# Kernel optimization log

Hardware: AMD Instinct MI355X
Metric: run time of the kernel (lower is better)

## Reference

```python
import jax, jax.numpy as jnp
import numpy as np

B, L, D, DEPTH, FF, VOCAB = 2, 2048, 1024, 4, 4096, 32000

def setup_inputs():
    key = jax.random.key(0)
    ks = jax.random.split(key, 16)
    n = lambda k, s, sc: jax.random.normal(k, s, dtype=jnp.float32) * sc
    sw = 0.01 / float(np.sqrt(D))  # xavier_normal with gain 0.01 on square dims
    return dict(
        tokens=jax.random.randint(ks[0], (B, L), 0, VOCAB),
        emb=n(ks[1], (VOCAB, D), 0.02),
        Wz=n(ks[2], (DEPTH, D, D), sw), bz=jnp.zeros((DEPTH, D)),
        Wza=n(ks[3], (DEPTH, D, D), sw), bza=jnp.zeros((DEPTH, D)),
        Wy=n(ks[4], (DEPTH, D, D), sw), by=jnp.zeros((DEPTH, D)),
        Wya=n(ks[5], (DEPTH, D, D), sw), bya=jnp.zeros((DEPTH, D)),
        lc_re=n(ks[6], (DEPTH, D), 1.0), lc_im=n(ks[7], (DEPTH, D), 1.0),
        g_in=jnp.ones((DEPTH, D)), g_sc=jnp.ones((DEPTH, D)), g_ffn=jnp.ones((DEPTH, D)),
        Wf=n(ks[8], (DEPTH, D, FF), 0.02), bf=jnp.zeros((DEPTH, FF)),
        Wfa=n(ks[9], (DEPTH, D, FF), 0.02), bfa=jnp.zeros((DEPTH, FF)),
        Wfo=n(ks[10], (DEPTH, FF, D), 0.02), bfo=jnp.zeros((DEPTH, D)),
        ln_w=jnp.ones((D,)), ln_b=jnp.zeros((D,)),
        Wout=n(ks[11], (D, VOCAB), 0.02), bout=jnp.zeros((VOCAB,)),
    )

def _silu(x):
    return x * jax.nn.sigmoid(x)

def _rms(x, w, eps=1e-6):
    return x * jax.lax.rsqrt(jnp.mean(x * x, axis=-1, keepdims=True) + eps) * w

def reference(tokens, emb, Wz, bz, Wza, bza, Wy, by, Wya, bya, lc_re, lc_im,
              g_in, g_sc, g_ffn, Wf, bf, Wfa, bfa, Wfo, bfo, ln_w, ln_b, Wout, bout):
    Bq, Lq = tokens.shape
    # Embedding with max_norm=1: torch renorms accessed rows to norm <= 1
    e = emb[tokens]
    nrm = jnp.linalg.norm(e, axis=-1, keepdims=True)
    x = e * jnp.minimum(1.0, 1.0 / jnp.maximum(nrm, 1e-7))
    # Decaying phazor kernel (shared across layers; phazor_angle_scale is a fixed buffer)
    angle = jnp.power(0.001, jnp.linspace(0.0, 1.0, D))
    ln_ph = (1e-5 + 1j * angle).astype(jnp.complex64)      # [D]
    t = jnp.arange(Lq, dtype=jnp.float32)
    ph = jnp.exp(t[:, None] * ln_ph[None, :])              # [L, D] complex
    pf = jnp.fft.fft(ph, n=2 * Lq, axis=0)                 # [2L, D]
    decay = jnp.exp(ln_ph)                                 # [D]
    for i in range(DEPTH):
        # --- SConv sublayer (pre-RMSNorm + residual) ---
        xr = x
        xn = _rms(x, g_sc[i])
        z = (xn @ Wz[i] + bz[i]) * _silu(xn @ Wza[i] + bza[i])
        zf = jnp.fft.fft(z.astype(jnp.complex64), n=2 * Lq, axis=1)
        h = jnp.fft.ifft(zf * pf[None], axis=1)[:, :Lq]    # inner-chunk causal decaying conv
        lc = (lc_re[i] + 1j * lc_im[i]).astype(jnp.complex64)
        h = h + lc[None, None, :] * ph[None] * decay[None, None, :]  # cross-chunk state carry
        y = (_rms(h.real, g_in[i]) @ Wy[i] + by[i]) * _silu(xn @ Wya[i] + bya[i])
        x = xr + y
        # --- FFN SwiGLU sublayer (pre-RMSNorm + residual) ---
        xr = x
        xn = _rms(x, g_ffn[i])
        x = xr + ((xn @ Wf[i] + bf[i]) * _silu(xn @ Wfa[i] + bfa[i])) @ Wfo[i] + bfo[i]
    # Final LayerNorm + vocab projection
    mu = jnp.mean(x, axis=-1, keepdims=True)
    var = jnp.mean((x - mu) ** 2, axis=-1, keepdims=True)
    x = (x - mu) * jax.lax.rsqrt(var + 1e-5) * ln_w + ln_b
    return x @ Wout + bout
```

## Files before the change

kernel.cpp:

```cpp
#include <hip/hip_runtime.h>
#include <math.h>

typedef __attribute__((ext_vector_type(8))) short bf16x8;
typedef __attribute__((ext_vector_type(4))) float f32x4;

#define DEVI __device__ __forceinline__

DEVI short f2bf(float f) {
  unsigned u = __builtin_bit_cast(unsigned, f);
  return (short)((u + 0x7fffu + ((u >> 16) & 1u)) >> 16);
}
DEVI float bf2f(short s) {
  unsigned u = ((unsigned)(unsigned short)s) << 16;
  return __builtin_bit_cast(float, u);
}

DEVI float silu_f(float v) { return v / (1.0f + expf(-v)); }

DEVI void async16(const void* g, void* l) {
  __builtin_amdgcn_global_load_lds(
      (const __attribute__((address_space(1))) void*)g,
      (__attribute__((address_space(3))) void*)l, 16, 0, 0);
}

template <int N>
DEVI void waitvm() { asm volatile("s_waitcnt vmcnt(%0)" ::"i"(N) : "memory"); }
DEVI void barrier_mem() { asm volatile("s_barrier" ::: "memory"); }
DEVI void lgkm0_sb() {
  asm volatile("s_waitcnt lgkmcnt(0)" ::: "memory");
  __builtin_amdgcn_sched_barrier(0);
}

template <int NROWT>
DEVI void tile_map(int* bx, int* by) {
  const int nwg = gridDim.x;
  const int lin = blockIdx.x;
  const int q = nwg >> 3;
  const int wgid = (lin & 7) * q + (lin >> 3);
  *by = wgid % NROWT;
  *bx = wgid / NROWT;
}

#define SWZ(r) ((ks ^ (((r) >> 1) & 3)) << 4)

__global__ __launch_bounds__(512, 2) void gemm8_k(const short* __restrict__ A,
                                                  const short* __restrict__ BT,
                                                  const float* __restrict__ bias,
                                                  float* __restrict__ outp,
                                                  int N, int K) {
  __shared__ __align__(16) char lds[2 * 65536];
  int bx, by;
  tile_map<16>(&bx, &by);
  const int row0 = by << 8, col0 = bx << 8;
  const int t = threadIdx.x, w = t >> 6, lane = t & 63;
  const int wm = w >> 2, wn = w & 3;
  const int lr = lane & 15, ks = lane >> 4;
  f32x4 acc[8][4] = {};

  const int sslot = (t & 3) ^ ((t >> 3) & 3);
  const char* gA = (const char*)A + ((size_t)(row0 + (t >> 2)) * K) * 2 + sslot * 16;
  const char* gB = (const char*)BT + ((size_t)(col0 + (t >> 2)) * K) * 2 + sslot * 16;
  const size_t cstep = (size_t)K << 8;
  const int t16 = t << 4;

  const int nkt = K >> 6;

#define SA8(nb, kt, s)                                                        \
  {                                                                           \
    const size_t co = (size_t)(kt) * 128 + (s) * 64;                          \
    async16(gA + co, (nb) + (s) * 16384 + t16);                               \
    async16(gA + cstep + co, (nb) + (s) * 16384 + 8192 + t16);                \
  }
#define SB8(nb, kt, s)                                                        \
  {                                                                           \
    const size_t co = (size_t)(kt) * 128 + (s) * 64;                          \
    async16(gB + co, (nb) + 32768 + (s) * 16384 + t16);                       \
    async16(gB + cstep + co, (nb) + 32768 + (s) * 16384 + 8192 + t16);        \
  }
#define RB8(s)                                                                \
  _Pragma("unroll") for (int n = 0; n < 4; ++n) {                             \
    const int rb = (wn << 6) + (n << 4) + lr;                                 \
    bfr[n] = *(const bf16x8*)(base + 32768 + (s) * 16384 + rb * 64 + SWZ(rb)); \
  }
#define RA8(s, mh)                                                            \
  _Pragma("unroll") for (int m = 0; m < 4; ++m) {                             \
    const int r = (wm << 7) + (mh) * 64 + (m << 4) + lr;                      \
    af[m] = *(const bf16x8*)(base + (s) * 16384 + r * 64 + SWZ(r));           \
  }
#define MM8(mh)                                                               \
  __builtin_amdgcn_s_setprio(1);                                              \
  _Pragma("unroll") for (int m = 0; m < 4; ++m)                               \
  _Pragma("unroll") for (int n = 0; n < 4; ++n)                               \
      acc[(mh) * 4 + m][n] = __builtin_amdgcn_mfma_f32_16x16x32_bf16(         \
          af[m], bfr[n], acc[(mh) * 4 + m][n], 0, 0, 0);                      \
  __builtin_amdgcn_s_setprio(0);                                              \
  __builtin_amdgcn_sched_barrier(0);

  {
    char* nb = lds;
    SA8(nb, 0, 0); SB8(nb, 0, 0); SA8(nb, 0, 1); SB8(nb, 0, 1);
  }

  for (int kt = 0; kt < nkt; ++kt) {
    const int ktn = kt + 1;
    const char* base = lds + (kt & 1) * 65536;
    char* nb = lds + (ktn & 1) * 65536;
    bf16x8 af[4], bfr[4];
    waitvm<4>();
    barrier_mem();
    if (ktn < nkt) SA8(nb, ktn, 0);
    RB8(0); RA8(0, 0);
    lgkm0_sb();
    MM8(0);
    barrier_mem();
    if (ktn < nkt) SB8(nb, ktn, 0);
    RA8(0, 1);
    lgkm0_sb();
    MM8(1);
    if (ktn < nkt) waitvm<4>();
    else waitvm<0>();
    barrier_mem();
    if (ktn < nkt) SA8(nb, ktn, 1);
    RB8(1); RA8(1, 0);
    lgkm0_sb();
    MM8(0);
    barrier_mem();
    if (ktn < nkt) SB8(nb, ktn, 1);
    RA8(1, 1);
    lgkm0_sb();
    MM8(1);
  }

  const int orow = row0 + (wm << 7) + (ks << 2);
  const int ocol = col0 + (wn << 6) + lr;
#pragma unroll
  for (int mf = 0; mf < 8; ++mf) {
#pragma unroll
    for (int n = 0; n < 4; ++n) {
      const int c = ocol + (n << 4);
      const float bv = bias[c];
#pragma unroll
      for (int i = 0; i < 4; ++i) {
        const int r = orow + (mf << 4) + i;
        outp[(size_t)r * N + c] = acc[mf][n][i] + bv;
      }
    }
  }
#undef SA8
#undef SB8
#undef RB8
#undef RA8
#undef MM8
}

__global__ __launch_bounds__(512, 2) void dual8_k(const short* __restrict__ A,
                                                  const short* __restrict__ BT1,
                                                  const short* __restrict__ BT2,
                                                  const float* __restrict__ bias1,
                                                  const float* __restrict__ bias2,
                                                  short* __restrict__ outp,
                                                  int N, int K) {
  __shared__ __align__(16) char lds[2 * 32768];
  int bx, by;
  tile_map<16>(&bx, &by);
  const int row0 = by << 8, col0 = bx << 7;
  const int t = threadIdx.x, w = t >> 6, lane = t & 63;
  const int wm = w >> 1, wn = w & 1;
  const int lr = lane & 15, ks = lane >> 4;
  f32x4 acc1[4][4] = {}, acc2[4][4] = {};

  const int sslot = (t & 3) ^ ((t >> 3) & 3);
  const char* gA = (const char*)A + ((size_t)(row0 + (t >> 2)) * K) * 2 + sslot * 16;
  const char* gB1 = (const char*)BT1 + ((size_t)(col0 + (t >> 2)) * K) * 2 + sslot * 16;
  const char* gB2 = (const char*)BT2 + ((size_t)(col0 + (t >> 2)) * K) * 2 + sslot * 16;
  const size_t cstep = (size_t)K << 8;
  const int t16 = t << 4;
  const int nkt = K >> 5;

#define SAD(nb, kt)                                                           \
  {                                                                           \
    const size_t co = (size_t)(kt) * 64;                                      \
    async16(gA + co, (nb) + t16);                                             \
    async16(gA + cstep + co, (nb) + 8192 + t16);                              \
  }
#define SB1D(nb, kt) async16(gB1 + (size_t)(kt) * 64, (nb) + 16384 + t16)
#define SB2D(nb, kt) async16(gB2 + (size_t)(kt) * 64, (nb) + 24576 + t16)

  { char* nb = lds; SAD(nb, 0); SB1D(nb, 0); SB2D(nb, 0); }

  for (int kt = 0; kt < nkt; ++kt) {
    const int ktn = kt + 1;
    const char* base = lds + (kt & 1) * 32768;
    char* nb = lds + (ktn & 1) * 32768;
    bf16x8 af[4], bfr[4];
    waitvm<1>();
    barrier_mem();
    if (ktn < nkt) { SAD(nb, ktn); SB1D(nb, ktn); }
#pragma unroll
    for (int n = 0; n < 4; ++n) {
      const int rb = (wn << 6) + (n << 4) + lr;
      bfr[n] = *(const bf16x8*)(base + 16384 + rb * 64 + SWZ(rb));
    }
#pragma unroll
    for (int m = 0; m < 4; ++m) {
      const int r = (wm << 6) + (m << 4) + lr;
      af[m] = *(const bf16x8*)(base + r * 64 + SWZ(r));
    }
    lgkm0_sb();
    __builtin_amdgcn_s_setprio(1);
#pragma unroll
    for (int m = 0; m < 4; ++m)
#pragma unroll
      for (int n = 0; n < 4; ++n)
        acc1[m][n] = __builtin_amdgcn_mfma_f32_16x16x32_bf16(af[m], bfr[n], acc1[m][n], 0, 0, 0);
    __builtin_amdgcn_s_setprio(0);
    __builtin_amdgcn_sched_barrier(0);
    if (ktn < nkt) waitvm<3>();
    else waitvm<0>();
    barrier_mem();
    if (ktn < nkt) SB2D(nb, ktn);
#pragma unroll
    for (int n = 0; n < 4; ++n) {
      const int rb = (wn << 6) + (n << 4) + lr;
      bfr[n] = *(const bf16x8*)(base + 24576 + rb * 64 + SWZ(rb));
    }
    lgkm0_sb();
    __builtin_amdgcn_s_setprio(1);
#pragma unroll
    for (int m = 0; m < 4; ++m)
#pragma unroll
      for (int n = 0; n < 4; ++n)
        acc2[m][n] = __builtin_amdgcn_mfma_f32_16x16x32_bf16(af[m], bfr[n], acc2[m][n], 0, 0, 0);
    __builtin_amdgcn_s_setprio(0);
    __builtin_amdgcn_sched_barrier(0);
  }

  const int orow = row0 + (wm << 6) + (ks << 2);
  const int ocol = col0 + (wn << 6) + lr;
#pragma unroll
  for (int m = 0; m < 4; ++m) {
#pragma unroll
    for (int n = 0; n < 4; ++n) {
      const int c = ocol + (n << 4);
      const float bv1 = bias1[c], bv2 = bias2[c];
#pragma unroll
      for (int i = 0; i < 4; ++i) {
        const int r = orow + (m << 4) + i;
        outp[(size_t)r * N + c] = f2bf((acc1[m][n][i] + bv1) * silu_f(acc2[m][n][i] + bv2));
      }
    }
  }
#undef SAD
#undef SB1D
#undef SB2D
}

__global__ __launch_bounds__(256, 2) void triple_k(const short* __restrict__ A,
                                                   const short* __restrict__ BT1,
                                                   const short* __restrict__ BT2,
                                                   const short* __restrict__ BT3,
                                                   const float* __restrict__ b1,
                                                   const float* __restrict__ b2,
                                                   const float* __restrict__ b3,
                                                   short* __restrict__ zout,
                                                   short* __restrict__ yaout,
                                                   int N, int K) {
  constexpr int PBB = 28672;
  __shared__ __align__(16) char lds[2 * PBB];
  int bx, by;
  tile_map<64>(&bx, &by);
  const int row0 = by << 6, col0 = bx << 7;
  const int t = threadIdx.x, w = t >> 6, lane = t & 63;
  const int wr = w >> 1, wc = w & 1;
  const int lr = lane & 15, ks = lane >> 4;
  f32x4 acc1[2][4] = {}, acc2[2][4] = {}, acc3[2][4] = {};

  const int sslot = (t & 3) ^ ((t >> 3) & 3);
  const char* gA = (const char*)A + ((size_t)(row0 + (t >> 2)) * K) * 2 + sslot * 16;
  const size_t brow = ((size_t)(col0 + (t >> 2)) * K) * 2 + sslot * 16;
  const char* gB1 = (const char*)BT1 + brow;
  const char* gB2 = (const char*)BT2 + brow;
  const char* gB3 = (const char*)BT3 + brow;
  const size_t cstep = (size_t)K * 128;
  const int t16 = t << 4;
  const int nkt = K >> 5;

#define STA(nb, kt) async16(gA + (size_t)(kt) * 64, (nb) + t16)
#define STB(nb, kt, gp, off)                                                  \
  {                                                                           \
    const size_t co = (size_t)(kt) * 64;                                      \
    async16((gp) + co, (nb) + (off) + t16);                                   \
    async16((gp) + cstep + co, (nb) + (off) + 4096 + t16);                    \
  }

  { char* nb = lds; STA(nb, 0); STB(nb, 0, gB1, 4096); STB(nb, 0, gB2, 12288); STB(nb, 0, gB3, 20480); }

  for (int kt = 0; kt < nkt; ++kt) {
    const int ktn = kt + 1;
    const char* base = lds + (kt & 1) * PBB;
    char* nb = lds + (ktn & 1) * PBB;
    bf16x8 af[2], bfr[4];
    waitvm<0>();
    barrier_mem();
    if (ktn < nkt) { STA(nb, ktn); STB(nb, ktn, gB1, 4096); }
#pragma unroll
    for (int m = 0; m < 2; ++m) {
      const int r = (wr << 5) + (m << 4) + lr;
      af[m] = *(const bf16x8*)(base + r * 64 + SWZ(r));
    }
#pragma unroll
    for (int n = 0; n < 4; ++n) {
      const int rb = (wc << 6) + (n << 4) + lr;
      bfr[n] = *(const bf16x8*)(base + 4096 + rb * 64 + SWZ(rb));
    }
    lgkm0_sb();
    __builtin_amdgcn_s_setprio(1);
#pragma unroll
    for (int m = 0; m < 2; ++m)
#pragma unroll
      for (int n = 0; n < 4; ++n)
        acc1[m][n] = __builtin_amdgcn_mfma_f32_16x16x32_bf16(af[m], bfr[n], acc1[m][n], 0, 0, 0);
    __builtin_amdgcn_s_setprio(0);
    __builtin_amdgcn_sched_barrier(0);
    if (ktn < nkt) STB(nb, ktn, gB2, 12288);
#pragma unroll
    for (int n = 0; n < 4; ++n) {
      const int rb = (wc << 6) + (n << 4) + lr;
      bfr[n] = *(const bf16x8*)(base + 12288 + rb * 64 + SWZ(rb));
    }
    lgkm0_sb();
    __builtin_amdgcn_s_setprio(1);
#pragma unroll
    for (int m = 0; m < 2; ++m)
#pragma unroll
      for (int n = 0; n < 4; ++n)
        acc2[m][n] = __builtin_amdgcn_mfma_f32_16x16x32_bf16(af[m], bfr[n], acc2[m][n], 0, 0, 0);
    __builtin_amdgcn_s_setprio(0);
    __builtin_amdgcn_sched_barrier(0);
    if (ktn < nkt) STB(nb, ktn, gB3, 20480);
#pragma unroll
    for (int n = 0; n < 4; ++n) {
      const int rb = (wc << 6) + (n << 4) + lr;
      bfr[n] = *(const bf16x8*)(base + 20480 + rb * 64 + SWZ(rb));
    }
    lgkm0_sb();
    __builtin_amdgcn_s_setprio(1);
#pragma unroll
    for (int m = 0; m < 2; ++m)
#pragma unroll
      for (int n = 0; n < 4; ++n)
        acc3[m][n] = __builtin_amdgcn_mfma_f32_16x16x32_bf16(af[m], bfr[n], acc3[m][n], 0, 0, 0);
    __builtin_amdgcn_s_setprio(0);
    __builtin_amdgcn_sched_barrier(0);
  }

  const int orow = row0 + (wr << 5) + (ks << 2);
  const int ocol = col0 + (wc << 6) + lr;
#pragma unroll
  for (int m = 0; m < 2; ++m) {
#pragma unroll
    for (int n = 0; n < 4; ++n) {
      const int c = ocol + (n << 4);
      const float bv1 = b1[c], bv2 = b2[c], bv3 = b3[c];
#pragma unroll
      for (int i = 0; i < 4; ++i) {
        const int r = orow + (m << 4) + i;
        const size_t idx = (size_t)r * N + c;
        zout[idx] = f2bf((acc1[m][n][i] + bv1) * silu_f(acc2[m][n][i] + bv2));
        yaout[idx] = f2bf(acc3[m][n][i] + bv3);
      }
    }
  }
#undef STA
#undef STB
}

template <int MODE, int BM, int BN, int WM, int WN, int NBUF>
__global__ __launch_bounds__(256, 2) void gemm_k(const short* __restrict__ A,
                                                 const short* __restrict__ BT,
                                                 const float* __restrict__ bias,
                                                 const short* __restrict__ aux,
                                                 void* __restrict__ outp,
                                                 int N, int K) {
  constexpr int MF = WM / 16, NF = WN / 16;
  constexpr int NWN = BN / WN;
  constexpr int PBB = (BM + BN) * 64;
  constexpr int DEPTH = NBUF - 1;
  constexpr int L = (BM + BN) / 64;
  static_assert((BM / WM) * (BN / WN) == 4, "4 waves");
  __shared__ __align__(16) char lds[NBUF * PBB];
  int bx, by;
  tile_map<4096 / BM>(&bx, &by);
  const int row0 = by * BM, col0 = bx * BN;
  const int t = threadIdx.x, w = t >> 6, lane = t & 63;
  const int wr = w / NWN, wc = w % NWN;
  f32x4 acc[MF][NF] = {};

  const int sslot = (t & 3) ^ ((t >> 3) & 3);
  const char* gA0 = (const char*)A + ((size_t)(row0 + (t >> 2)) * K) * 2 + sslot * 16;
  const char* gB0 = (const char*)BT + ((size_t)(col0 + (t >> 2)) * K) * 2 + sslot * 16;
  const size_t ccstep = (size_t)K * 128;
  const int wb = w << 10;
  const int lr = lane & 15, ks = lane >> 4;

  const int NIT = K >> 5;
  auto stage = [&](int buf, int it) {
    char* dst = lds + buf * PBB;
    const size_t io = (size_t)it * 64;
#pragma unroll
    for (int cc = 0; cc < BM / 64; ++cc)
      async16(gA0 + io + cc * ccstep, dst + cc * 4096 + wb);
#pragma unroll
    for (int cc = 0; cc < BN / 64; ++cc)
      async16(gB0 + io + cc * ccstep, dst + BM * 64 + cc * 4096 + wb);
  };

#pragma unroll
  for (int pit = 0; pit < DEPTH; ++pit) stage(pit, pit);

  for (int it = 0; it < NIT; ++it) {
    const int rem = NIT - it;
    if (rem >= DEPTH + 1) waitvm<L * (DEPTH - 1)>();
    else if (rem >= 2) waitvm<L>();
    else waitvm<0>();
    barrier_mem();
    if (it + DEPTH < NIT) stage((it + DEPTH) % NBUF, it + DEPTH);
    const char* base = lds + (it % NBUF) * PBB;
    bf16x8 af[MF], bfr[NF];
#pragma unroll
    for (int m = 0; m < MF; ++m) {
      const int r = wr * WM + m * 16 + lr;
      af[m] = *(const bf16x8*)(base + r * 64 + SWZ(r));
    }
#pragma unroll
    for (int n = 0; n < NF; ++n) {
      const int r = wc * WN + n * 16 + lr;
      bfr[n] = *(const bf16x8*)(base + BM * 64 + r * 64 + SWZ(r));
    }
    lgkm0_sb();
    __builtin_amdgcn_s_setprio(1);
#pragma unroll
    for (int m = 0; m < MF; ++m)
#pragma unroll
      for (int n = 0; n < NF; ++n)
        acc[m][n] = __builtin_amdgcn_mfma_f32_16x16x32_bf16(af[m], bfr[n], acc[m][n], 0, 0, 0);
    __builtin_amdgcn_s_setprio(0);
    __builtin_amdgcn_sched_barrier(0);
  }

  const int orow = row0 + wr * WM + (ks << 2);
  const int ocol = col0 + wc * WN + lr;
#pragma unroll
  for (int m = 0; m < MF; ++m) {
#pragma unroll
    for (int n = 0; n < NF; ++n) {
      const int c = ocol + (n << 4);
      const float bv = bias[c];
#pragma unroll
      for (int i = 0; i < 4; ++i) {
        const int r = orow + (m << 4) + i;
        const size_t idx = (size_t)r * N + c;
        float v = acc[m][n][i] + bv;
        if (MODE == 0) ((float*)outp)[idx] = v;
        else if (MODE == 3) ((float*)outp)[idx] += v * silu_f(bf2f(aux[idx]));
        else ((float*)outp)[idx] += v;
      }
    }
  }
}

__global__ __launch_bounds__(256) void transp_k(const float* __restrict__ W,
                                                short* __restrict__ WT,
                                                int R, int C) {
  __shared__ float tile[32][33];
  const size_t moff = (size_t)blockIdx.z * R * C;
  const float* Wp = W + moff;
  short* Tp = WT + moff;
  const int c0 = blockIdx.x << 5, r0 = blockIdx.y << 5;
  const int tx = threadIdx.x, ty = threadIdx.y;
#pragma unroll
  for (int i = 0; i < 4; ++i)
    tile[ty + 8 * i][tx] = Wp[(size_t)(r0 + ty + 8 * i) * C + (c0 + tx)];
  __syncthreads();
#pragma unroll
  for (int i = 0; i < 4; ++i)
    Tp[(size_t)(c0 + ty + 8 * i) * R + (r0 + tx)] = f2bf(tile[tx][ty + 8 * i]);
}

__global__ __launch_bounds__(256) void embed_k(const int* __restrict__ tok,
                                               const float* __restrict__ emb,
                                               float* __restrict__ x) {
  const int row = blockIdx.x, t = threadIdx.x, w = t >> 6, lane = t & 63;
  const int token = tok[row];
  float4 v = ((const float4*)(emb + (size_t)token * 1024))[t];
  float ss = v.x * v.x + v.y * v.y + v.z * v.z + v.w * v.w;
#pragma unroll
  for (int off = 32; off; off >>= 1) ss += __shfl_xor(ss, off, 64);
  __shared__ float red[4];
  if (lane == 0) red[w] = ss;
  __syncthreads();
  const float nrm = sqrtf(red[0] + red[1] + red[2] + red[3]);
  const float sc = fminf(1.0f, 1.0f / fmaxf(nrm, 1e-7f));
  v.x *= sc; v.y *= sc; v.z *= sc; v.w *= sc;
  ((float4*)(x + (size_t)row * 1024))[t] = v;
}

template <int BF>
__global__ __launch_bounds__(256) void rms_k(const void* __restrict__ xin,
                                             const float* __restrict__ g,
                                             short* __restrict__ o) {
  const int row = blockIdx.x, t = threadIdx.x, w = t >> 6, lane = t & 63;
  float v0, v1, v2, v3;
  if (BF) {
    short4 s = ((const short4*)((const short*)xin + (size_t)row * 1024))[t];
    v0 = bf2f(s.x); v1 = bf2f(s.y); v2 = bf2f(s.z); v3 = bf2f(s.w);
  } else {
    float4 v = ((const float4*)((const float*)xin + (size_t)row * 1024))[t];
    v0 = v.x; v1 = v.y; v2 = v.z; v3 = v.w;
  }
  float ss = v0 * v0 + v1 * v1 + v2 * v2 + v3 * v3;
#pragma unroll
  for (int off = 32; off; off >>= 1) ss += __shfl_xor(ss, off, 64);
  __shared__ float red[4];
  if (lane == 0) red[w] = ss;
  __syncthreads();
  const float sc = rsqrtf((red[0] + red[1] + red[2] + red[3]) * (1.0f / 1024.0f) + 1e-6f);
  float4 gv = ((const float4*)g)[t];
  short4 ov = make_short4(f2bf(v0 * sc * gv.x), f2bf(v1 * sc * gv.y),
                          f2bf(v2 * sc * gv.z), f2bf(v3 * sc * gv.w));
  *(short4*)(o + (size_t)row * 1024 + 4 * t) = ov;
}

__global__ __launch_bounds__(256) void ln_k(const float* __restrict__ x,
                                            const float* __restrict__ lw,
                                            const float* __restrict__ lb,
                                            short* __restrict__ o) {
  const int row = blockIdx.x, t = threadIdx.x, w = t >> 6, lane = t & 63;
  float4 v = ((const float4*)(x + (size_t)row * 1024))[t];
  float s1 = v.x + v.y + v.z + v.w;
  float s2 = v.x * v.x + v.y * v.y + v.z * v.z + v.w * v.w;
#pragma unroll
  for (int off = 32; off; off >>= 1) {
    s1 += __shfl_xor(s1, off, 64);
    s2 += __shfl_xor(s2, off, 64);
  }
  __shared__ float red[8];
  if (lane == 0) { red[w] = s1; red[4 + w] = s2; }
  __syncthreads();
  const float mu = (red[0] + red[1] + red[2] + red[3]) * (1.0f / 1024.0f);
  const float ex2 = (red[4] + red[5] + red[6] + red[7]) * (1.0f / 1024.0f);
  const float rs = rsqrtf(ex2 - mu * mu + 1e-5f);
  float4 wv = ((const float4*)lw)[t];
  float4 bv = ((const float4*)lb)[t];
  short4 ov = make_short4(f2bf((v.x - mu) * rs * wv.x + bv.x),
                          f2bf((v.y - mu) * rs * wv.y + bv.y),
                          f2bf((v.z - mu) * rs * wv.z + bv.z),
                          f2bf((v.w - mu) * rs * wv.w + bv.w));
  *(short4*)(o + (size_t)row * 1024 + 4 * t) = ov;
}

DEVI void decay_of(int d, float* dr, float* di) {
  const float ang = powf(1e-3f, (float)d * (1.0f / 1023.0f));
  float sn, cs;
  sincosf(ang, &sn, &cs);
  const float mag = expf(1e-5f);
  *dr = mag * cs; *di = mag * sn;
}

__global__ __launch_bounds__(256) void s1_k(const short* __restrict__ z,
                                            float* __restrict__ Er, float* __restrict__ Ei) {
  const int d = (blockIdx.x << 8) + threadIdx.x;
  const int c = blockIdx.y, b = blockIdx.z;
  float dr, di;
  decay_of(d, &dr, &di);
  const short* zp = z + ((size_t)(b * 2048 + c * 64) << 10) + d;
  float sr = 0.0f, si = 0.0f;
  for (int k = 0; k < 64; ++k) {
    float zv = bf2f(zp[(size_t)k << 10]);
    float nr = dr * sr - di * si + zv;
    si = dr * si + di * sr;
    sr = nr;
  }
  const int idx = ((b << 5) + c) * 1024 + d;
  Er[idx] = sr; Ei[idx] = si;
}

__global__ __launch_bounds__(256) void s3_k(const short* __restrict__ z,
                                            const float* __restrict__ Er,
                                            const float* __restrict__ Ei,
                                            const float* __restrict__ lcre,
                                            const float* __restrict__ lcim,
                                            short* __restrict__ h) {
  const int d = (blockIdx.x << 8) + threadIdx.x;
  const int c = blockIdx.y, b = blockIdx.z;
  float dr, di;
  decay_of(d, &dr, &di);
  float ar = dr, ai = di;
#pragma unroll
  for (int q = 0; q < 6; ++q) { float nr = ar * ar - ai * ai; ai = 2.0f * ar * ai; ar = nr; }
  float sr = 0.0f, si = 0.0f;
  for (int cc = 0; cc < c; ++cc) {
    const int eidx = ((b << 5) + cc) * 1024 + d;
    const float er = Er[eidx], ei = Ei[eidx];
    const float nr = ar * sr - ai * si + er;
    si = ar * si + ai * sr + ei;
    sr = nr;
  }
  float wr = 1.0f, wi = 0.0f, br = ar, bi = ai;
  int e = c;
  while (e) {
    if (e & 1) { float nr = wr * br - wi * bi; wi = wr * bi + wi * br; wr = nr; }
    float nb = br * br - bi * bi; bi = 2.0f * br * bi; br = nb;
    e >>= 1;
  }
  { float nr = wr * dr - wi * di; wi = wr * di + wi * dr; wr = nr; }
  const float lr_ = lcre[d], li_ = lcim[d];
  const size_t base = ((size_t)(b * 2048 + c * 64) << 10) + d;
  for (int k = 0; k < 64; ++k) {
    const float zv = bf2f(z[base + ((size_t)k << 10)]);
    const float nr = dr * sr - di * si + zv;
    si = dr * si + di * sr;
    sr = nr;
    h[base + ((size_t)k << 10)] = f2bf(sr + lr_ * wr - li_ * wi);
    const float nw = wr * dr - wi * di;
    wi = wr * di + wi * dr;
    wr = nw;
  }
}

extern "C" void kernel_launch(void* const* d_in, const int* in_sizes, int n_in,
                              void* d_out, int out_size, void* d_ws, size_t ws_size,
                              hipStream_t stream) {
  const int* tokens = (const int*)d_in[0];
  const float* emb = (const float*)d_in[1];
  const float* Wz = (const float*)d_in[2];
  const float* bz = (const float*)d_in[3];
  const float* Wza = (const float*)d_in[4];
  const float* bza = (const float*)d_in[5];
  const float* Wy = (const float*)d_in[6];
  const float* by = (const float*)d_in[7];
  const float* Wya = (const float*)d_in[8];
  const float* bya = (const float*)d_in[9];
  const float* lc_re = (const float*)d_in[10];
  const float* lc_im = (const float*)d_in[11];
  const float* g_in = (const float*)d_in[12];
  const float* g_sc = (const float*)d_in[13];
  const float* g_ffn = (const float*)d_in[14];
  const float* Wf = (const float*)d_in[15];
  const float* bf = (const float*)d_in[16];
  const float* Wfa = (const float*)d_in[17];
  const float* bfa = (const float*)d_in[18];
  const float* Wfo = (const float*)d_in[19];
  const float* bfo = (const float*)d_in[20];
  const float* ln_w = (const float*)d_in[21];
  const float* ln_b = (const float*)d_in[22];
  const float* Wout = (const float*)d_in[23];
  const float* bout = (const float*)d_in[24];

  char* p = (char*)d_ws;
  float* xb = (float*)p;   p += (size_t)4096 * 1024 * 4;
  short* zb = (short*)p;   p += (size_t)4096 * 1024 * 2;
  short* hb = (short*)p;   p += (size_t)4096 * 1024 * 2;
  short* yab = (short*)p;  p += (size_t)4096 * 1024 * 2;
  float* Er = (float*)p;   p += (size_t)2 * 32 * 1024 * 4;
  float* Ei = (float*)p;   p += (size_t)2 * 32 * 1024 * 4;
  short* xnb = (short*)p;  p += (size_t)4096 * 1024 * 2;
  short* hnb = (short*)p;  p += (size_t)4096 * 1024 * 2;
  short* gb = (short*)p;   p += (size_t)4096 * 4096 * 2;
  short* WzT = (short*)p;  p += (size_t)4 * 1024 * 1024 * 2;
  short* WzaT = (short*)p; p += (size_t)4 * 1024 * 1024 * 2;
  short* WyT = (short*)p;  p += (size_t)4 * 1024 * 1024 * 2;
  short* WyaT = (short*)p; p += (size_t)4 * 1024 * 1024 * 2;
  short* WfT = (short*)p;  p += (size_t)4 * 1024 * 4096 * 2;
  short* WfaT = (short*)p; p += (size_t)4 * 1024 * 4096 * 2;
  short* WfoT = (short*)p; p += (size_t)4 * 1024 * 4096 * 2;
  short* WoutT = (short*)p; p += (size_t)32000 * 1024 * 2;

  const dim3 tb(32, 8);
  transp_k<<<dim3(32, 32, 4), tb, 0, stream>>>(Wz, WzT, 1024, 1024);
  transp_k<<<dim3(32, 32, 4), tb, 0, stream>>>(Wza, WzaT, 1024, 1024);
  transp_k<<<dim3(32, 32, 4), tb, 0, stream>>>(Wy, WyT, 1024, 1024);
  transp_k<<<dim3(32, 32, 4), tb, 0, stream>>>(Wya, WyaT, 1024, 1024);
  transp_k<<<dim3(128, 32, 4), tb, 0, stream>>>(Wf, WfT, 1024, 4096);
  transp_k<<<dim3(128, 32, 4), tb, 0, stream>>>(Wfa, WfaT, 1024, 4096);
  transp_k<<<dim3(32, 128, 4), tb, 0, stream>>>(Wfo, WfoT, 4096, 1024);
  transp_k<<<dim3(1000, 32, 1), tb, 0, stream>>>(Wout, WoutT, 1024, 32000);

  embed_k<<<4096, 256, 0, stream>>>(tokens, emb, xb);

  for (int i = 0; i < 4; ++i) {
    const size_t dd = (size_t)i * 1024 * 1024;
    const size_t dv = (size_t)i * 1024;
    const size_t dw = (size_t)i * 1024 * 4096;
    const size_t df = (size_t)i * 4096;
    rms_k<0><<<4096, 256, 0, stream>>>(xb, g_sc + dv, xnb);
    triple_k<<<512, 256, 0, stream>>>(xnb, WzT + dd, WzaT + dd, WyaT + dd,
                                      bz + dv, bza + dv, bya + dv, zb, yab, 1024, 1024);
    s1_k<<<dim3(4, 32, 2), 256, 0, stream>>>(zb, Er, Ei);
    s3_k<<<dim3(4, 32, 2), 256, 0, stream>>>(zb, Er, Ei, lc_re + dv, lc_im + dv, hb);
    rms_k<1><<<4096, 256, 0, stream>>>(hb, g_in + dv, hnb);
    gemm_k<3, 64, 128, 32, 64, 3><<<512, 256, 0, stream>>>(
        hnb, WyT + dd, by + dv, yab, xb, 1024, 1024);
    rms_k<0><<<4096, 256, 0, stream>>>(xb, g_ffn + dv, xnb);
    dual8_k<<<512, 512, 0, stream>>>(xnb, WfT + dw, WfaT + dw, bf + df, bfa + df,
                                     gb, 4096, 1024);
    gemm_k<4, 64, 128, 32, 64, 4><<<512, 256, 0, stream>>>(
        gb, WfoT + dw, bfo + dv, nullptr, xb, 1024, 4096);
  }

  ln_k<<<4096, 256, 0, stream>>>(xb, ln_w, ln_b, xnb);
  gemm8_k<<<2000, 512, 0, stream>>>(xnb, WoutT, bout, (float*)d_out, 32000, 1024);

  (void)in_sizes; (void)n_in; (void)out_size; (void)ws_size;
}
```

Measured before the change: 1.568 ms.

## Deepen GEMM prefetch to four-stage LDS ring and refine async waits

The main bf16 GEMM and the dual SwiGLU GEMM move from a double-buffered LDS pipeline to a four-slot ring with a K-step of 32, prefetching three tiles ahead. Their launch bounds drop to one workgroup per CU to fit the larger LDS footprint. The triple-output kernel replaces its full vmcnt(0) wait with partial waits and extra barriers, so later B loads can stay in flight. This aims to hide global-load latency behind MFMA work, at the cost of lower occupancy and more per-iteration barriers.

```diff
diff --git a/kernel.cpp b/kernel.cpp
--- a/kernel.cpp
+++ b/kernel.cpp
@@ -43,12 +43,12 @@
 
 #define SWZ(r) ((ks ^ (((r) >> 1) & 3)) << 4)
 
-__global__ __launch_bounds__(512, 2) void gemm8_k(const short* __restrict__ A,
+__global__ __launch_bounds__(512, 1) void gemm8_k(const short* __restrict__ A,
                                                   const short* __restrict__ BT,
                                                   const float* __restrict__ bias,
                                                   float* __restrict__ outp,
                                                   int N, int K) {
-  __shared__ __align__(16) char lds[2 * 65536];
+  __shared__ __align__(16) char lds[4 * 32768];
   int bx, by;
   tile_map<16>(&bx, &by);
   const int row0 = by << 8, col0 = bx << 8;
@@ -62,30 +62,29 @@
   const char* gB = (const char*)BT + ((size_t)(col0 + (t >> 2)) * K) * 2 + sslot * 16;
   const size_t cstep = (size_t)K << 8;
   const int t16 = t << 4;
-
-  const int nkt = K >> 6;
-
-#define SA8(nb, kt, s)                                                        \
+  const int nkt = K >> 5;
+
+#define SA8(nb, kt)                                                           \
   {                                                                           \
-    const size_t co = (size_t)(kt) * 128 + (s) * 64;                          \
-    async16(gA + co, (nb) + (s) * 16384 + t16);                               \
-    async16(gA + cstep + co, (nb) + (s) * 16384 + 8192 + t16);                \
-  }
-#define SB8(nb, kt, s)                                                        \
+    const size_t co = (size_t)(kt) << 6;                                      \
+    async16(gA + co, (nb) + t16);                                             \
+    async16(gA + cstep + co, (nb) + 8192 + t16);                              \
+  }
+#define SB8(nb, kt)                                                           \
   {                                                                           \
-    const size_t co = (size_t)(kt) * 128 + (s) * 64;                          \
-    async16(gB + co, (nb) + 32768 + (s) * 16384 + t16);                       \
-    async16(gB + cstep + co, (nb) + 32768 + (s) * 16384 + 8192 + t16);        \
-  }
-#define RB8(s)                                                                \
+    const size_t co = (size_t)(kt) << 6;                                      \
+    async16(gB + co, (nb) + 16384 + t16);                                     \
+    async16(gB + cstep + co, (nb) + 24576 + t16);                             \
+  }
+#define RB8()                                                                 \
   _Pragma("unroll") for (int n = 0; n < 4; ++n) {                             \
     const int rb = (wn << 6) + (n << 4) + lr;                                 \
-    bfr[n] = *(const bf16x8*)(base + 32768 + (s) * 16384 + rb * 64 + SWZ(rb)); \
-  }
-#define RA8(s, mh)                                                            \
+    bfr[n] = *(const bf16x8*)(base + 16384 + rb * 64 + SWZ(rb));              \
+  }
+#define RA8(mh)                                                               \
   _Pragma("unroll") for (int m = 0; m < 4; ++m) {                             \
-    const int r = (wm << 7) + (mh) * 64 + (m << 4) + lr;                      \
-    af[m] = *(const bf16x8*)(base + (s) * 16384 + r * 64 + SWZ(r));           \
+    const int r = (wm << 7) + ((mh) << 6) + (m << 4) + lr;                    \
+    af[m] = *(const bf16x8*)(base + r * 64 + SWZ(r));                         \
   }
 #define MM8(mh)                                                               \
   __builtin_amdgcn_s_setprio(1);                                              \
@@ -96,37 +95,26 @@
   __builtin_amdgcn_s_setprio(0);                                              \
   __builtin_amdgcn_sched_barrier(0);
 
-  {
-    char* nb = lds;
-    SA8(nb, 0, 0); SB8(nb, 0, 0); SA8(nb, 0, 1); SB8(nb, 0, 1);
-  }
+  SA8(lds, 0); SB8(lds, 0);
+  SA8(lds + 32768, 1); SB8(lds + 32768, 1);
+  SA8(lds + 65536, 2); SB8(lds + 65536, 2);
 
   for (int kt = 0; kt < nkt; ++kt) {
-    const int ktn = kt + 1;
-    const char* base = lds + (kt & 1) * 65536;
-    char* nb = lds + (ktn & 1) * 65536;
+    const char* base = lds + (kt & 3) * 32768;
+    char* nb = lds + ((kt + 3) & 3) * 32768;
+    const int rem = nkt - kt;
     bf16x8 af[4], bfr[4];
-    waitvm<4>();
+    if (rem > 2) waitvm<8>();
+    else if (rem == 2) waitvm<4>();
+    else waitvm<0>();
     barrier_mem();
-    if (ktn < nkt) SA8(nb, ktn, 0);
-    RB8(0); RA8(0, 0);
+    if (kt + 3 < nkt) SA8(nb, kt + 3);
+    RB8(); RA8(0);
     lgkm0_sb();
     MM8(0);
     barrier_mem();
-    if (ktn < nkt) SB8(nb, ktn, 0);
-    RA8(0, 1);
-    lgkm0_sb();
-    MM8(1);
-    if (ktn < nkt) waitvm<4>();
-    else waitvm<0>();
-    barrier_mem();
-    if (ktn < nkt) SA8(nb, ktn, 1);
-    RB8(1); RA8(1, 0);
-    lgkm0_sb();
-    MM8(0);
-    barrier_mem();
-    if (ktn < nkt) SB8(nb, ktn, 1);
-    RA8(1, 1);
+    if (kt + 3 < nkt) SB8(nb, kt + 3);
+    RA8(1);
     lgkm0_sb();
     MM8(1);
   }
@@ -153,14 +141,14 @@
 #undef MM8
 }
 
-__global__ __launch_bounds__(512, 2) void dual8_k(const short* __restrict__ A,
+__global__ __launch_bounds__(512, 1) void dual8_k(const short* __restrict__ A,
                                                   const short* __restrict__ BT1,
                                                   const short* __restrict__ BT2,
                                                   const float* __restrict__ bias1,
                                                   const float* __restrict__ bias2,
                                                   short* __restrict__ outp,
                                                   int N, int K) {
-  __shared__ __align__(16) char lds[2 * 32768];
+  __shared__ __align__(16) char lds[4 * 32768];
   int bx, by;
   tile_map<16>(&bx, &by);
   const int row0 = by << 8, col0 = bx << 7;
@@ -179,23 +167,27 @@
 
 #define SAD(nb, kt)                                                           \
   {                                                                           \
-    const size_t co = (size_t)(kt) * 64;                                      \
+    const size_t co = (size_t)(kt) << 6;                                      \
     async16(gA + co, (nb) + t16);                                             \
     async16(gA + cstep + co, (nb) + 8192 + t16);                              \
   }
-#define SB1D(nb, kt) async16(gB1 + (size_t)(kt) * 64, (nb) + 16384 + t16)
-#define SB2D(nb, kt) async16(gB2 + (size_t)(kt) * 64, (nb) + 24576 + t16)
-
-  { char* nb = lds; SAD(nb, 0); SB1D(nb, 0); SB2D(nb, 0); }
+#define SB1D(nb, kt) async16(gB1 + ((size_t)(kt) << 6), (nb) + 16384 + t16)
+#define SB2D(nb, kt) async16(gB2 + ((size_t)(kt) << 6), (nb) + 24576 + t16)
+
+  SAD(lds, 0); SB1D(lds, 0); SB2D(lds, 0);
+  SAD(lds + 32768, 1); SB1D(lds + 32768, 1); SB2D(lds + 32768, 1);
+  SAD(lds + 65536, 2); SB1D(lds + 65536, 2); SB2D(lds + 65536, 2);
 
   for (int kt = 0; kt < nkt; ++kt) {
-    const int ktn = kt + 1;
-    const char* base = lds + (kt & 1) * 32768;
-    char* nb = lds + (ktn & 1) * 32768;
+    const char* base = lds + (kt & 3) * 32768;
+    char* nb = lds + ((kt + 3) & 3) * 32768;
+    const int rem = nkt - kt;
     bf16x8 af[4], bfr[4];
-    waitvm<1>();
+    if (rem > 2) waitvm<8>();
+    else if (rem == 2) waitvm<4>();
+    else waitvm<0>();
     barrier_mem();
-    if (ktn < nkt) { SAD(nb, ktn); SB1D(nb, ktn); }
+    if (kt + 3 < nkt) SAD(nb, kt + 3);
 #pragma unroll
     for (int n = 0; n < 4; ++n) {
       const int rb = (wn << 6) + (n << 4) + lr;
@@ -215,10 +207,8 @@
         acc1[m][n] = __builtin_amdgcn_mfma_f32_16x16x32_bf16(af[m], bfr[n], acc1[m][n], 0, 0, 0);
     __builtin_amdgcn_s_setprio(0);
     __builtin_amdgcn_sched_barrier(0);
-    if (ktn < nkt) waitvm<3>();
-    else waitvm<0>();
     barrier_mem();
-    if (ktn < nkt) SB2D(nb, ktn);
+    if (kt + 3 < nkt) { SB1D(nb, kt + 3); SB2D(nb, kt + 3); }
 #pragma unroll
     for (int n = 0; n < 4; ++n) {
       const int rb = (wn << 6) + (n << 4) + lr;
@@ -300,7 +290,7 @@
     const char* base = lds + (kt & 1) * PBB;
     char* nb = lds + (ktn & 1) * PBB;
     bf16x8 af[2], bfr[4];
-    waitvm<0>();
+    waitvm<4>();
     barrier_mem();
     if (ktn < nkt) { STA(nb, ktn); STB(nb, ktn, gB1, 4096); }
 #pragma unroll
@@ -322,6 +312,9 @@
         acc1[m][n] = __builtin_amdgcn_mfma_f32_16x16x32_bf16(af[m], bfr[n], acc1[m][n], 0, 0, 0);
     __builtin_amdgcn_s_setprio(0);
     __builtin_amdgcn_sched_barrier(0);
+    if (ktn < nkt) waitvm<5>();
+    else waitvm<2>();
+    barrier_mem();
     if (ktn < nkt) STB(nb, ktn, gB2, 12288);
 #pragma unroll
     for (int n = 0; n < 4; ++n) {
@@ -337,6 +330,9 @@
         acc2[m][n] = __builtin_amdgcn_mfma_f32_16x16x32_bf16(af[m], bfr[n], acc2[m][n], 0, 0, 0);
     __builtin_amdgcn_s_setprio(0);
     __builtin_amdgcn_sched_barrier(0);
+    if (ktn < nkt) waitvm<5>();
+    else waitvm<0>();
+    barrier_mem();
     if (ktn < nkt) STB(nb, ktn, gB3, 20480);
 #pragma unroll
     for (int n = 0; n < 4; ++n) {
```

Result: no change. 1.561 ms (-0.5%).
